# Kernel tuning notes

Measured on AMD Instinct MI355X. Metric: run time of the kernel, lower is better.

## Reference

```python
import jax, jax.numpy as jnp
import numpy as np
import math

STRIDES = [4, 8, 16, 32, 64]
SCALES  = [32, 64, 128, 256, 512]
RATIOS  = [2.0, 1.0, 0.5]
GRIDS   = [(200, 304), (100, 152), (50, 76), (25, 38), (13, 19)]  # 800x1216 canvas
LSZ     = [gh * gw * 3 for gh, gw in GRIDS]                        # anchors per level
PRE_NMS_K = [min(1000, n) for n in LSZ]                            # select_by_score (1000, lsz)
IMG_H, IMG_W = 800, 1216
BBOX_CLAMP = math.log(1000.0 / 16.0)
IOU_TH = 0.7
MAX_OUT = 1000
MIN_SIZE = 1e-2
LEVEL_OFFSET = 1e4  # batched-NMS level separation offset


def _make_priors():
    # post.get_priors with loc='corner': anchor centers at stride*i (no +0.5)
    out = []
    for st, (gh, gw), sc in zip(STRIDES, GRIDS, SCALES):
        anc = []
        for r in RATIOS:  # make_anchors_rounded: 1 scale x 3 ratios, rounded
            h = sc * np.sqrt(r)
            w = sc / np.sqrt(r)
            anc.append(np.round(np.array([-w / 2, -h / 2, w / 2, h / 2])))
        anc = np.stack(anc)  # [3,4]
        ys = (np.arange(gh) * st).astype(np.float32)
        xs = (np.arange(gw) * st).astype(np.float32)
        yy, xx = np.meshgrid(ys, xs, indexing='ij')
        shifts = np.stack([xx, yy, xx, yy], axis=-1).reshape(-1, 1, 4)  # [gh*gw,1,4]
        out.append((shifts + anc[None].astype(np.float32)).reshape(-1, 4))
    return np.concatenate(out).astype(np.float32)  # [A,4]


def setup_inputs() -> dict:
    key = jax.random.key(0)
    k1, k2 = jax.random.split(key)
    B, A = 16, sum(LSZ)
    reg = jax.random.normal(k1, (B, A, 4), dtype=jnp.float32) * 0.5  # box deltas
    obj = jax.random.normal(k2, (B, A, 1), dtype=jnp.float32)        # objectness logits
    priors = jnp.asarray(_make_priors())
    return {"reg": reg, "obj": obj, "priors": priors}


def _nms(boxes, init_keep):
    # sequential NMS over score-sorted boxes; boxes already level-offset. [N,4]
    N = boxes.shape[0]
    areas = jnp.clip(boxes[:, 2] - boxes[:, 0], 0) * jnp.clip(boxes[:, 3] - boxes[:, 1], 0)
    rng = jnp.arange(N)

    def body(i, keep):
        b = boxes[i]
        xx1 = jnp.maximum(b[0], boxes[:, 0])
        yy1 = jnp.maximum(b[1], boxes[:, 1])
        xx2 = jnp.minimum(b[2], boxes[:, 2])
        yy2 = jnp.minimum(b[3], boxes[:, 3])
        inter = jnp.clip(xx2 - xx1, 0) * jnp.clip(yy2 - yy1, 0)
        iou = inter / (areas[i] + areas - inter + 1e-9)
        sup = (iou > IOU_TH) & (rng > i) & keep[i]
        return keep & ~sup

    return jax.lax.fori_loop(0, N, body, init_keep)


def reference(reg, obj, priors):
    B = reg.shape[0]
    scores = jax.nn.sigmoid(obj[..., 0])  # [B,A]

    # per-level top-k selection (select_by_score with (1000, lsz))
    off = 0
    idxs, scs, levs = [], [], []
    for l, (n, k) in enumerate(zip(LSZ, PRE_NMS_K)):
        sv, si = jax.lax.top_k(scores[:, off:off + n], k)
        idxs.append(si + off)
        scs.append(sv)
        levs.append(np.full(k, l, np.int32))
        off += n
    idx = jnp.concatenate(idxs, axis=1)       # [B,N] global anchor indices
    sc = jnp.concatenate(scs, axis=1)         # [B,N]
    levels = jnp.asarray(np.concatenate(levs))  # [N]

    reg_s = jnp.take_along_axis(reg, idx[..., None], axis=1)  # [B,N,4]
    pri_s = priors[idx]                                        # [B,N,4]

    # decode_boxes, settings=(1, 1, log(1000/16))
    pw = pri_s[..., 2] - pri_s[..., 0]
    ph = pri_s[..., 3] - pri_s[..., 1]
    pcx = pri_s[..., 0] + 0.5 * pw
    pcy = pri_s[..., 1] + 0.5 * ph
    dx, dy = reg_s[..., 0], reg_s[..., 1]
    dw = jnp.minimum(reg_s[..., 2], BBOX_CLAMP)
    dh = jnp.minimum(reg_s[..., 3], BBOX_CLAMP)
    cx = dx * pw + pcx
    cy = dy * ph + pcy
    w = pw * jnp.exp(dw)
    h = ph * jnp.exp(dh)
    boxes = jnp.stack([cx - 0.5 * w, cy - 0.5 * h, cx + 0.5 * w, cy + 0.5 * h], axis=-1)

    # clamp_to_canvas
    boxes = jnp.stack([
        jnp.clip(boxes[..., 0], 0, IMG_W), jnp.clip(boxes[..., 1], 0, IMG_H),
        jnp.clip(boxes[..., 2], 0, IMG_W), jnp.clip(boxes[..., 3], 0, IMG_H)], axis=-1)

    # remove_small
    small_ok = ((boxes[..., 2] - boxes[..., 0]) > MIN_SIZE) & ((boxes[..., 3] - boxes[..., 1]) > MIN_SIZE)

    # global score-descending order for NMS
    order = jnp.argsort(-sc, axis=1)
    boxes = jnp.take_along_axis(boxes, order[..., None], axis=1)
    sc = jnp.take_along_axis(sc, order, axis=1)
    small_ok = jnp.take_along_axis(small_ok, order, axis=1)
    lev = jnp.take_along_axis(jnp.broadcast_to(levels, sc.shape), order, axis=1)

    # per-level batched NMS via coordinate offset; NMS decisions are non-differentiable
    boxes_off = jax.lax.stop_gradient(boxes) + lev[..., None].astype(boxes.dtype) * LEVEL_OFFSET
    keep = jax.vmap(_nms)(boxes_off, small_ok)  # [B,N] bool

    # take first MAX_OUT kept (already score-sorted), pad with zeros
    rank = jnp.cumsum(keep, axis=1) - 1
    pos = jnp.where(keep & (rank < MAX_OUT), rank, MAX_OUT)  # dump slot MAX_OUT
    out_b = jax.vmap(lambda p, b: jnp.zeros((MAX_OUT + 1, 4), b.dtype).at[p].set(b))(pos, boxes)[:, :MAX_OUT]
    out_s = jax.vmap(lambda p, s: jnp.zeros((MAX_OUT + 1,), s.dtype).at[p].set(s))(pos, sc)[:, :MAX_OUT]
    return jnp.concatenate([out_b, out_s[..., None]], axis=-1)  # [B,1000,5]
```

## Files before the change

### kernel.cpp

```cpp
#include <hip/hip_runtime.h>

typedef unsigned int u32;
typedef unsigned short u16;
typedef unsigned long long u64;

#define NB 16
#define NA 242991
#define NSEL 4741

__device__ __constant__ int c_LN[5]   = {182400, 45600, 11400, 2850, 741};
__device__ __constant__ int c_LOFF[5] = {0, 182400, 228000, 239400, 242250};
__device__ __constant__ int c_LK[5]   = {1000, 1000, 1000, 1000, 741};
__device__ __constant__ int c_SOFF[5] = {0, 1000, 2000, 3000, 4000};
__device__ __constant__ int c_CST[5]  = {0, 64, 80, 84, 85};
__device__ __constant__ int c_CCN[5]  = {64, 16, 4, 1, 1};


__device__ __forceinline__ float xla_tanhf(float x) {
#pragma clang fp contract(off)
  float t = fminf(fmaxf(x, -9.0f), 9.0f);
  float x2 = t * t;
  float p = -2.76076847742355e-16f;
  p = p * x2 + 2.00018790482477e-13f;
  p = p * x2 + -8.60467152213735e-11f;
  p = p * x2 + 5.12229709037114e-08f;
  p = p * x2 + 1.48572235717979e-05f;
  p = p * x2 + 6.37261928875436e-04f;
  p = p * x2 + 4.89352455891786e-03f;
  p = t * p;
  float q = 1.19825839466702e-06f;
  q = q * x2 + 1.18534705686654e-04f;
  q = q * x2 + 2.26843463243900e-03f;
  q = q * x2 + 4.89352518554385e-03f;
  float r = p / q;
  return (fabsf(x) < 0.0004f) ? x : r;
}

__device__ __forceinline__ float ref_sigmoid(float x) {
#pragma clang fp contract(off)
  float t = 0.5f * x;
  float th = xla_tanhf(t);
  return 0.5f + 0.5f * th;
}

__device__ __forceinline__ float xla_expf(float x) {
#pragma clang fp contract(off)
  float fx = x * 1.44269504088896341f + 0.5f;
  fx = floorf(fx);
  float tmp = fx * 0.693359375f;
  float z = fx * -2.12194440e-4f;
  float r = x - tmp;
  r = r - z;
  float r2 = r * r;
  float y = 1.9875691500e-4f;
  y = y * r + 1.3981999507e-3f;
  y = y * r + 8.3334519073e-3f;
  y = y * r + 4.1665795894e-2f;
  y = y * r + 1.6666665459e-1f;
  y = y * r + 5.0000001201e-1f;
  y = y * r2 + r;
  y = y + 1.0f;
  int k = (int)fx;
  float two_k = __uint_as_float((u32)((k + 127) << 23));
  return y * two_k;
}

__device__ __forceinline__ void chunk_map(int c, int& l, int& base, int& n) {
  if (c < 64)      { l = 0; base = c * 2850;                 n = 2850; }
  else if (c < 80) { l = 1; base = 182400 + (c - 64) * 2850; n = 2850; }
  else if (c < 84) { l = 2; base = 228000 + (c - 80) * 2850; n = 2850; }
  else if (c == 84){ l = 3; base = 239400;                   n = 2850; }
  else             { l = 4; base = 242250;                   n = 741;  }
}


__global__ void __launch_bounds__(256) k_hist(const float* __restrict__ obj,
                                              u16* __restrict__ ghist) {
  const int c = blockIdx.x, b = blockIdx.y;
  int l, base, n;
  chunk_map(c, l, base, n);
  __shared__ u32 h[4096];
  for (int i = threadIdx.x; i < 4096; i += 256) h[i] = 0;
  __syncthreads();
  const float* src = obj + (size_t)b * NA + base;
  for (int i = threadIdx.x; i < n; i += 256) {
    float s = ref_sigmoid(src[i]);
    atomicAdd(&h[__float_as_uint(s) >> 18], 1u);
  }
  __syncthreads();
  u32* gh = (u32*)(ghist + ((size_t)b * 86 + c) * 4096);
  for (int i = threadIdx.x; i < 2048; i += 256)
    gh[i] = (h[2 * i] & 0xFFFFu) | (h[2 * i + 1] << 16);
}


__global__ void __launch_bounds__(1024) k_thresh(const u16* __restrict__ ghist,
                                                 int2* __restrict__ binfo,
                                                 u32* __restrict__ ctrs) {
  const int l = blockIdx.x, b = blockIdx.y, t = threadIdx.x;
  const int K = c_LK[l];
  const int bl = b * 5 + l;
  if (t == 0) { ctrs[bl] = 0; ctrs[80 + bl] = 0; }
  __shared__ u32 scan[1024];
  __shared__ int sh_b;
  __shared__ u32 sh_G;
  u32 h0 = 0, h1 = 0, h2 = 0, h3 = 0;
  const int cs = c_CST[l], cn = c_CCN[l];
  const u16* base = ghist + (size_t)b * 86 * 4096 + 4 * t;
  for (int cc = 0; cc < cn; ++cc) {
    uint2 v = *(const uint2*)(base + (size_t)(cs + cc) * 4096);
    h0 += v.x & 0xFFFFu; h1 += v.x >> 16;
    h2 += v.y & 0xFFFFu; h3 += v.y >> 16;
  }
  u32 loc = h0 + h1 + h2 + h3;
  scan[t] = loc;
  __syncthreads();
  for (int d = 1; d < 1024; d <<= 1) {
    u32 v = (t + d < 1024) ? scan[t + d] : 0u;
    __syncthreads();
    scan[t] += v;
    __syncthreads();
  }
  u32 S = scan[t];
  u32 above = S - loc;
  if (S >= (u32)K && above < (u32)K) {
    u32 cacc = above;
    u32 cn2 = cacc + h3;
    if (cn2 >= (u32)K) { sh_b = 4 * t + 3; sh_G = cacc; }
    else {
      cacc = cn2; cn2 = cacc + h2;
      if (cn2 >= (u32)K) { sh_b = 4 * t + 2; sh_G = cacc; }
      else {
        cacc = cn2; cn2 = cacc + h1;
        if (cn2 >= (u32)K) { sh_b = 4 * t + 1; sh_G = cacc; }
        else { cacc = cn2; sh_b = 4 * t; sh_G = cacc; }
      }
    }
  }
  __syncthreads();
  if (t == 0) binfo[bl] = make_int2(sh_b, (int)sh_G);
}


__global__ void __launch_bounds__(256) k_emit(const float* __restrict__ obj,
                                              const int2* __restrict__ binfo,
                                              u64* __restrict__ skey,
                                              u64* __restrict__ candg,
                                              u32* __restrict__ ctrs) {
  const int c = blockIdx.x, b = blockIdx.y;
  int l, base, n;
  chunk_map(c, l, base, n);
  const int bl = b * 5 + l;
  const int bstar = binfo[bl].x;
  const float* src = obj + (size_t)b * NA + base;

  __shared__ u64 bufD[2880];
  __shared__ u64 bufC[2880];
  __shared__ u32 cntD, cntC, gbD, gbC;
  if (threadIdx.x == 0) { cntD = 0; cntC = 0; }
  __syncthreads();

  const int lane = (int)threadIdx.x & 63;
  const u64 lmask_lt = (lane == 0) ? 0ull : ((~0ull) >> (64 - lane));
  const int iters = (n + 255) >> 8;
  for (int it = 0; it < iters; ++it) {
    int i = it * 256 + (int)threadIdx.x;
    bool valid = i < n;
    float s = ref_sigmoid(valid ? src[i] : 0.0f);
    u32 bits = __float_as_uint(s);
    int bin = (int)(bits >> 18);
    bool isD = valid && (bin > bstar);
    bool isC = valid && (bin == bstar);
    u64 mD = __ballot(isD);
    u64 mC = __ballot(isC);
    u32 bD = 0, bC = 0;
    if (lane == 0) {
      if (mD) bD = atomicAdd(&cntD, (u32)__popcll(mD));
      if (mC) bC = atomicAdd(&cntC, (u32)__popcll(mC));
    }
    bD = (u32)__shfl((int)bD, 0, 64);
    bC = (u32)__shfl((int)bC, 0, 64);
    u64 key = ((u64)(bits ^ 0xFFFFFFFFu) << 32) | (u32)(base + i);
    if (isD) bufD[bD + (u32)__popcll(mD & lmask_lt)] = key;
    if (isC) bufC[bC + (u32)__popcll(mC & lmask_lt)] = key;
  }
  __syncthreads();
  if (threadIdx.x == 0) {
    gbD = atomicAdd(&ctrs[bl], cntD);
    gbC = atomicAdd(&ctrs[80 + bl], cntC);
  }
  __syncthreads();
  const u32 nD = cntD, nC = cntC, gD = gbD, gC = gbC;
  u64* dstD = skey + (size_t)b * NSEL + c_SOFF[l] + gD;
  for (u32 i = threadIdx.x; i < nD; i += 256) dstD[i] = bufD[i];
  u64* dstC = candg + (size_t)bl * 2048;
  for (u32 i = threadIdx.x; i < nC; i += 256) {
    u32 p = gC + i;
    if (p < 2048) dstC[p] = bufC[i];
  }
}


__device__ __forceinline__ u64 shflx64(u64 v, int d) {
  u32 lo = (u32)v, hi = (u32)(v >> 32);
  lo = (u32)__shfl_xor((int)lo, d, 64);
  hi = (u32)__shfl_xor((int)hi, d, 64);
  return ((u64)hi << 32) | (u64)lo;
}

__global__ void __launch_bounds__(1024) k_selsort(
    const u64* __restrict__ candg, const int2* __restrict__ binfo,
    const u32* __restrict__ ctrs, u64* __restrict__ skey,
    const float* __restrict__ reg, const float* __restrict__ priors,
    float* __restrict__ boxes, float* __restrict__ scoref,
    float* __restrict__ nmsbox, u64* __restrict__ sow) {
  const int l = blockIdx.x, b = blockIdx.y, t = threadIdx.x;
  const int bl = b * 5 + l;
  const int K = c_LK[l];
  const int G = binfo[bl].y;
  u32 cc = ctrs[80 + bl];
  if (cc > 2048) cc = 2048;
  __shared__ u64 sm[4096];
  __shared__ u64 sh_sow[16];
  if (t < 16) sh_sow[t] = 0ull;
  const u64* seg = skey + (size_t)b * NSEL + c_SOFF[l];
  const u64* cnd = candg + (size_t)bl * 2048;

  const int i0 = 4 * t;
  auto ld = [&](int i) -> u64 {
    if (i < G) return seg[i];
    int ci = i - G;
    return (ci < (int)cc) ? cnd[ci] : ~0ull;
  };
  u64 v0 = ld(i0), v1 = ld(i0 + 1), v2 = ld(i0 + 2), v3 = ld(i0 + 3);

  auto cs = [](u64& a, u64& b2, bool up) {
    if ((a > b2) == up) { u64 x = a; a = b2; b2 = x; }
  };

  cs(v0, v1, true);
  cs(v2, v3, false);
  {
    bool up = ((i0 & 4) == 0);
    cs(v0, v2, up); cs(v1, v3, up);
    cs(v0, v1, up); cs(v2, v3, up);
  }
  for (int k = 8; k <= 4096; k <<= 1) {
    const bool up = ((i0 & k) == 0);
    for (int j = k >> 1; j >= 256; j >>= 1) {
      sm[t] = v0; sm[1024 + t] = v1; sm[2048 + t] = v2; sm[3072 + t] = v3;
      __syncthreads();
      const int u = t ^ (j >> 2);
      u64 o0 = sm[u], o1 = sm[1024 + u], o2 = sm[2048 + u], o3 = sm[3072 + u];
      const bool keepmin = (((i0 & j) == 0) == up);
      v0 = keepmin ? (v0 < o0 ? v0 : o0) : (v0 > o0 ? v0 : o0);
      v1 = keepmin ? (v1 < o1 ? v1 : o1) : (v1 > o1 ? v1 : o1);
      v2 = keepmin ? (v2 < o2 ? v2 : o2) : (v2 > o2 ? v2 : o2);
      v3 = keepmin ? (v3 < o3 ? v3 : o3) : (v3 > o3 ? v3 : o3);
      __syncthreads();
    }
    int jstart = (k >> 1) < 128 ? (k >> 1) : 128;
    for (int j = jstart; j >= 4; j >>= 1) {
      const int d = j >> 2;
      const bool keepmin = (((t & d) == 0) == up);
      u64 o0 = shflx64(v0, d);
      u64 o1 = shflx64(v1, d);
      u64 o2 = shflx64(v2, d);
      u64 o3 = shflx64(v3, d);
      v0 = keepmin ? (v0 < o0 ? v0 : o0) : (v0 > o0 ? v0 : o0);
      v1 = keepmin ? (v1 < o1 ? v1 : o1) : (v1 > o1 ? v1 : o1);
      v2 = keepmin ? (v2 < o2 ? v2 : o2) : (v2 > o2 ? v2 : o2);
      v3 = keepmin ? (v3 < o3 ? v3 : o3) : (v3 > o3 ? v3 : o3);
    }
    cs(v0, v2, up); cs(v1, v3, up);
    cs(v0, v1, up); cs(v2, v3, up);
  }

  u64* dst = skey + (size_t)b * NSEL + c_SOFF[l];

  {
#pragma clang fp contract(off)
    const float lf = (float)l * 10000.0f;
    u64 kv[4] = {v0, v1, v2, v3};
#pragma unroll
    for (int e = 0; e < 4; ++e) {
      int r = i0 + e;
      if (r < K) {
        u64 kk = kv[e];
        dst[r] = kk;
        u32 idx = (u32)kk;
        if (idx >= (u32)NA) idx = NA - 1;
        u32 bits = (u32)(kk >> 32) ^ 0xFFFFFFFFu;
        float s = __uint_as_float(bits);
        float4 r4 = ((const float4*)reg)[(size_t)b * NA + idx];
        float4 q4 = ((const float4*)priors)[idx];
        float pw = q4.z - q4.x;
        float ph = q4.w - q4.y;
        float pcx = q4.x + 0.5f * pw;
        float pcy = q4.y + 0.5f * ph;
        float dw = fminf(r4.z, 4.135166556742356f);
        float dh = fminf(r4.w, 4.135166556742356f);
        float cx = r4.x * pw + pcx;
        float cy = r4.y * ph + pcy;
        float w = pw * xla_expf(dw);
        float h = ph * xla_expf(dh);
        float x1 = cx - 0.5f * w;
        float y1 = cy - 0.5f * h;
        float x2 = cx + 0.5f * w;
        float y2 = cy + 0.5f * h;
        x1 = fminf(fmaxf(x1, 0.0f), 1216.0f);
        y1 = fminf(fmaxf(y1, 0.0f), 800.0f);
        x2 = fminf(fmaxf(x2, 0.0f), 1216.0f);
        y2 = fminf(fmaxf(y2, 0.0f), 800.0f);
        bool ok = ((x2 - x1) > 0.01f) && ((y2 - y1) > 0.01f);
        int sidx = c_SOFF[l] + r;
        ((float4*)boxes)[(size_t)b * NSEL + sidx] = make_float4(x1, y1, x2, y2);
        scoref[(size_t)b * NSEL + sidx] = s;
        ((float4*)nmsbox)[(size_t)(b * 5 + l) * 1000 + r] =
            make_float4(x1 + lf, y1 + lf, x2 + lf, y2 + lf);
        if (ok) atomicOr(&sh_sow[r >> 6], 1ull << (r & 63));
      }
    }
  }
  __syncthreads();
  if (t < 16) sow[(size_t)b * 80 + l * 16 + t] = sh_sow[t];
}


__device__ __forceinline__ void tile_map(int k, int& l, int& ti, int& tj) {
  int W;
  if (k < 544) { l = k / 136; k -= l * 136; W = 16; }
  else         { l = 4; k -= 544; W = 12; }
  int a = 0;
  while (k >= W - a) { k -= W - a; a++; }
  ti = a; tj = a + k;
}

__global__ void __launch_bounds__(256) k_nms_build(const float* __restrict__ nmsbox,
                                                   u64* __restrict__ mk) {
#pragma clang fp contract(off)
  const int b = blockIdx.y;
  const int wv = (int)threadIdx.x >> 6;
  const int tid = blockIdx.x * 4 + wv;
  __shared__ float4 cbox[4][64];
  __shared__ float car[4][64];
  if (tid >= 622) return;
  const int lane = (int)threadIdx.x & 63;
  int l, ti, tj;
  tile_map(tid, l, ti, tj);
  const int N = c_LK[l];
  const int bl = b * 5 + l;
  const float4* src = (const float4*)(nmsbox + (size_t)bl * 4000);
  const int i = ti * 64 + lane;
  const int j = tj * 64 + lane;
  const int il = (i < N) ? i : (N - 1);
  const int jl = (j < N) ? j : (N - 1);
  float4 rb = src[il];
  float4 cb0 = src[jl];
  float ra = fmaxf(rb.z - rb.x, 0.0f) * fmaxf(rb.w - rb.y, 0.0f);
  float ca0 = fmaxf(cb0.z - cb0.x, 0.0f) * fmaxf(cb0.w - cb0.y, 0.0f);
  cbox[wv][lane] = cb0;
  car[wv][lane] = ca0;
  u32 mlo = 0u, mhi = 0u;
  const double M = 0.7000000178813934326171875;
#pragma unroll
  for (int c = 0; c < 64; ++c) {
    float4 cb = cbox[wv][c];
    float aj = car[wv][c];
    float xx1 = fmaxf(rb.x, cb.x);
    float yy1 = fmaxf(rb.y, cb.y);
    float xx2 = fminf(rb.z, cb.z);
    float yy2 = fminf(rb.w, cb.w);
    float inter = fmaxf(xx2 - xx1, 0.0f) * fmaxf(yy2 - yy1, 0.0f);
    float den = ((ra + aj) - inter) + 1e-9f;
    bool sup = ((double)inter >= M * (double)den);
    if (c < 32) mlo |= sup ? (1u << c) : 0u;
    else        mhi |= sup ? (1u << (c - 32)) : 0u;
  }
  u64 m = ((u64)mhi << 32) | (u64)mlo;
  if (ti == tj) m &= (lane == 63) ? 0ull : (~0ull << (lane + 1));
  int nc = N - tj * 64;
  if (nc < 64) m &= (1ull << nc) - 1ull;
  if (i < N) mk[(size_t)bl * 16000 + (size_t)tj * 1000 + i] = m;
}


__global__ void __launch_bounds__(1024) k_nms_scan(const u64* __restrict__ mk,
                                                   const u64* __restrict__ sow,
                                                   u64* __restrict__ keepw) {
  const int bl = blockIdx.x;
  const int b = bl / 5, l = bl % 5;
  const int N = c_LK[l];
  const int W = (N + 63) >> 6;
  const int lane = (int)threadIdx.x & 63;
  const int w = (int)threadIdx.x >> 6;
  const bool act = (w < W);
  __shared__ u64 sh_kept[16];

  const u64* rowp = mk + (size_t)bl * 16000 + (size_t)w * 1000;
  u64 acc = act ? ~sow[(size_t)b * 80 + l * 16 + w] : 0ull;

  u64 diag = 0ull;
  if (act) {
    int rd = w * 64 + lane;
    if (rd < N) diag = rowp[rd];
  }
  u64 nxt = (act && w > 0) ? rowp[lane] : 0ull;

  for (int g = 0; g < 16; ++g) {
    if (g >= W) break;
    u64 cur = nxt;
    if (act && w > g + 1) {
      int r = (g + 1) * 64 + lane;
      nxt = (r < N) ? rowp[r] : 0ull;
    } else {
      nxt = 0ull;
    }
    if (w == g) {
      u64 sup = acc;
      u64 pend = __ballot(diag != 0) & ~sup;
      while (pend) {
        int i = __builtin_ctzll(pend);
        u64 rr = __shfl(diag, i, 64);
        sup |= rr;
        pend &= ~sup;
        pend &= ~(1ull << i);
      }
      acc = sup;
      if (lane == 0) sh_kept[g] = ~sup;
    }
    __syncthreads();
    if (act && w > g) {
      u64 K = sh_kept[g];
      u64 c = ((K >> lane) & 1ull) ? cur : 0ull;
#pragma unroll
      for (int d = 1; d < 64; d <<= 1) c |= __shfl_xor(c, d, 64);
      acc |= c;
    }
    __syncthreads();
  }
  if (act && lane == 0) keepw[(size_t)b * 80 + l * 16 + w] = ~acc;
}


__global__ void __launch_bounds__(1024) k_out(const float* __restrict__ boxes,
                                              const float* __restrict__ scoref,
                                              const u64* __restrict__ skey,
                                              const u64* __restrict__ keepw,
                                              float* __restrict__ out) {
  const int l = blockIdx.x, b = blockIdx.y, t = threadIdx.x;
  __shared__ u64 sk[NSEL];
  __shared__ u64 kw[80];
  __shared__ u32 pp[5][17];
  __shared__ u32 sh_T;
  for (int i = t; i < NSEL; i += 1024) sk[i] = skey[(size_t)b * NSEL + i];
  if (t < 80) {
    int l2 = t >> 4, w = t & 15;
    int W = (c_LK[l2] + 63) >> 6;
    kw[t] = (w < W) ? keepw[(size_t)b * 80 + t] : 0ull;
  }
  __syncthreads();
  if (t < 5) {
    u32 acc = 0;
    pp[t][0] = 0;
    for (int w = 0; w < 16; ++w) {
      acc += (u32)__popcll(kw[t * 16 + w]);
      pp[t][w + 1] = acc;
    }
  }
  __syncthreads();
  if (t == 0) sh_T = pp[0][16] + pp[1][16] + pp[2][16] + pp[3][16] + pp[4][16];
  __syncthreads();
  const u32 T = sh_T;
  const int K = c_LK[l];

  for (int r = t; r < K; r += 1024) {
    int s = c_SOFF[l] + r;
    u64 word = kw[l * 16 + (r >> 6)];
    if ((word >> (r & 63)) & 1ull) {
      u32 rank = pp[l][r >> 6] +
                 (u32)__popcll(word & ((r & 63) ? ((1ull << (r & 63)) - 1ull) : 0ull));
      u64 key = sk[s];
#pragma unroll
      for (int l2 = 0; l2 < 5; ++l2) {
        if (l2 == l) continue;
        int lo = 0, hi = c_LK[l2];
        const int base2 = c_SOFF[l2];
        while (lo < hi) {
          int mid = (lo + hi) >> 1;
          if (sk[base2 + mid] < key) lo = mid + 1; else hi = mid;
        }
        u64 w2 = kw[l2 * 16 + (lo >> 6)];
        rank += pp[l2][lo >> 6] +
                (u32)__popcll(w2 & ((lo & 63) ? ((1ull << (lo & 63)) - 1ull) : 0ull));
      }
      if (rank < 1000u) {
        float4 bo = ((const float4*)boxes)[(size_t)b * NSEL + s];
        float* o = out + ((size_t)b * 1000 + rank) * 5;
        o[0] = bo.x; o[1] = bo.y; o[2] = bo.z; o[3] = bo.w;
        o[4] = scoref[(size_t)b * NSEL + s];
      }
    }
  }
  if (l == 0) {
    u32 start = (T < 1000u) ? T : 1000u;
    for (u32 i = start + t; i < 1000u; i += 1024u) {
      float* o = out + ((size_t)b * 1000 + i) * 5;
      o[0] = 0.0f; o[1] = 0.0f; o[2] = 0.0f; o[3] = 0.0f; o[4] = 0.0f;
    }
  }
}


extern "C" void kernel_launch(void* const* d_in, const int* in_sizes, int n_in,
                              void* d_out, int out_size, void* d_ws, size_t ws_size,
                              hipStream_t stream) {
  const float* reg = (const float*)d_in[0];
  const float* obj = (const float*)d_in[1];
  const float* priors = (const float*)d_in[2];
  float* out = (float*)d_out;

  char* ws = (char*)d_ws;
  size_t off = 0;
  auto alloc = [&](size_t bytes) {
    size_t r = off;
    off += (bytes + 255) & ~(size_t)255;
    return r;
  };
  u16* ghist = (u16*)(ws + alloc((size_t)NB * 86 * 4096 * 2));
  u32* ctrs = (u32*)(ws + alloc(160 * 4));
  int2* binfo = (int2*)(ws + alloc(80 * 8));
  u64* candg = (u64*)(ws + alloc((size_t)80 * 2048 * 8));
  u64* skey = (u64*)(ws + alloc((size_t)NB * NSEL * 8));
  float* boxes = (float*)(ws + alloc((size_t)NB * NSEL * 16));
  float* scoref = (float*)(ws + alloc((size_t)NB * NSEL * 4));
  float* nmsbox = (float*)(ws + alloc((size_t)NB * 5 * 1000 * 16));
  u64* sow = (u64*)(ws + alloc((size_t)NB * 80 * 8));
  u64* keepw = (u64*)(ws + alloc((size_t)NB * 80 * 8));
  u64* mk = (u64*)(ws + alloc((size_t)80 * 1000 * 16 * 8));

  k_hist<<<dim3(86, NB), 256, 0, stream>>>(obj, ghist);
  k_thresh<<<dim3(5, NB), 1024, 0, stream>>>(ghist, binfo, ctrs);
  k_emit<<<dim3(86, NB), 256, 0, stream>>>(obj, binfo, skey, candg, ctrs);
  k_selsort<<<dim3(5, NB), 1024, 0, stream>>>(candg, binfo, ctrs, skey, reg,
                                              priors, boxes, scoref, nmsbox, sow);
  k_nms_build<<<dim3(156, NB), 256, 0, stream>>>(nmsbox, mk);
  k_nms_scan<<<dim3(80), 1024, 0, stream>>>(mk, sow, keepw);
  k_out<<<dim3(5, NB), 1024, 0, stream>>>(boxes, scoref, skey, keepw, out);
}
```

Before: 120.8 us.

## Pack emit counters, shrink bitonic sort size, skip non-overlapping IoU columns

The emit kernel packs the D and C per-wave counts into a single 16/16-bit shared atomic, so there is one LDS atomic per wave iteration instead of two. The selection sort now picks a 2048-element network when the candidates fit, which idles half the threads and drops one merge stage. The NMS mask kernel skips the double-precision IoU test for any column where no lane in the wave has a positive intersection. The packed counters assume per-block counts stay below 65536, and the wave-uniform branch adds a ballot for every column.

```diff
diff --git a/kernel.cpp b/kernel.cpp
--- a/kernel.cpp
+++ b/kernel.cpp
@@ -156,8 +156,8 @@
 
   __shared__ u64 bufD[2880];
   __shared__ u64 bufC[2880];
-  __shared__ u32 cntD, cntC, gbD, gbC;
-  if (threadIdx.x == 0) { cntD = 0; cntC = 0; }
+  __shared__ u32 cntDC, gbD, gbC;
+  if (threadIdx.x == 0) cntDC = 0;
   __syncthreads();
 
   const int lane = (int)threadIdx.x & 63;
@@ -173,24 +173,24 @@
     bool isC = valid && (bin == bstar);
     u64 mD = __ballot(isD);
     u64 mC = __ballot(isC);
-    u32 bD = 0, bC = 0;
+    u32 bDC = 0;
     if (lane == 0) {
-      if (mD) bD = atomicAdd(&cntD, (u32)__popcll(mD));
-      if (mC) bC = atomicAdd(&cntC, (u32)__popcll(mC));
-    }
-    bD = (u32)__shfl((int)bD, 0, 64);
-    bC = (u32)__shfl((int)bC, 0, 64);
+      u32 add = (u32)__popcll(mD) | ((u32)__popcll(mC) << 16);
+      if (add) bDC = atomicAdd(&cntDC, add);
+    }
+    bDC = (u32)__shfl((int)bDC, 0, 64);
     u64 key = ((u64)(bits ^ 0xFFFFFFFFu) << 32) | (u32)(base + i);
-    if (isD) bufD[bD + (u32)__popcll(mD & lmask_lt)] = key;
-    if (isC) bufC[bC + (u32)__popcll(mC & lmask_lt)] = key;
-  }
-  __syncthreads();
+    if (isD) bufD[(bDC & 0xFFFFu) + (u32)__popcll(mD & lmask_lt)] = key;
+    if (isC) bufC[(bDC >> 16) + (u32)__popcll(mC & lmask_lt)] = key;
+  }
+  __syncthreads();
+  const u32 nD = cntDC & 0xFFFFu, nC = cntDC >> 16;
   if (threadIdx.x == 0) {
-    gbD = atomicAdd(&ctrs[bl], cntD);
-    gbC = atomicAdd(&ctrs[80 + bl], cntC);
-  }
-  __syncthreads();
-  const u32 nD = cntD, nC = cntC, gD = gbD, gC = gbC;
+    gbD = atomicAdd(&ctrs[bl], nD);
+    gbC = atomicAdd(&ctrs[80 + bl], nC);
+  }
+  __syncthreads();
+  const u32 gD = gbD, gC = gbC;
   u64* dstD = skey + (size_t)b * NSEL + c_SOFF[l] + gD;
   for (u32 i = threadIdx.x; i < nD; i += 256) dstD[i] = bufD[i];
   u64* dstC = candg + (size_t)bl * 2048;
@@ -226,54 +226,66 @@
   const u64* seg = skey + (size_t)b * NSEL + c_SOFF[l];
   const u64* cnd = candg + (size_t)bl * 2048;
 
+  const int total = G + (int)cc;
+  const int NS = (total <= 2048) ? 2048 : 4096;
+  const int Q = NS >> 2;
+  const bool act = (t < Q);
   const int i0 = 4 * t;
-  auto ld = [&](int i) -> u64 {
-    if (i < G) return seg[i];
-    int ci = i - G;
-    return (ci < (int)cc) ? cnd[ci] : ~0ull;
-  };
-  u64 v0 = ld(i0), v1 = ld(i0 + 1), v2 = ld(i0 + 2), v3 = ld(i0 + 3);
+
+  u64 v0 = ~0ull, v1 = ~0ull, v2 = ~0ull, v3 = ~0ull;
+  if (act) {
+    auto ld = [&](int i) -> u64 {
+      if (i < G) return seg[i];
+      int ci = i - G;
+      return (ci < (int)cc) ? cnd[ci] : ~0ull;
+    };
+    v0 = ld(i0); v1 = ld(i0 + 1); v2 = ld(i0 + 2); v3 = ld(i0 + 3);
+  }
 
   auto cs = [](u64& a, u64& b2, bool up) {
     if ((a > b2) == up) { u64 x = a; a = b2; b2 = x; }
   };
 
-  cs(v0, v1, true);
-  cs(v2, v3, false);
-  {
+  if (act) {
+    cs(v0, v1, true);
+    cs(v2, v3, false);
     bool up = ((i0 & 4) == 0);
     cs(v0, v2, up); cs(v1, v3, up);
     cs(v0, v1, up); cs(v2, v3, up);
   }
-  for (int k = 8; k <= 4096; k <<= 1) {
+  for (int k = 8; k <= NS; k <<= 1) {
     const bool up = ((i0 & k) == 0);
     for (int j = k >> 1; j >= 256; j >>= 1) {
-      sm[t] = v0; sm[1024 + t] = v1; sm[2048 + t] = v2; sm[3072 + t] = v3;
+      if (act) { sm[t] = v0; sm[Q + t] = v1; sm[2 * Q + t] = v2; sm[3 * Q + t] = v3; }
       __syncthreads();
-      const int u = t ^ (j >> 2);
-      u64 o0 = sm[u], o1 = sm[1024 + u], o2 = sm[2048 + u], o3 = sm[3072 + u];
-      const bool keepmin = (((i0 & j) == 0) == up);
-      v0 = keepmin ? (v0 < o0 ? v0 : o0) : (v0 > o0 ? v0 : o0);
-      v1 = keepmin ? (v1 < o1 ? v1 : o1) : (v1 > o1 ? v1 : o1);
-      v2 = keepmin ? (v2 < o2 ? v2 : o2) : (v2 > o2 ? v2 : o2);
-      v3 = keepmin ? (v3 < o3 ? v3 : o3) : (v3 > o3 ? v3 : o3);
+      if (act) {
+        const int u = t ^ (j >> 2);
+        u64 o0 = sm[u], o1 = sm[Q + u], o2 = sm[2 * Q + u], o3 = sm[3 * Q + u];
+        const bool keepmin = (((i0 & j) == 0) == up);
+        v0 = keepmin ? (v0 < o0 ? v0 : o0) : (v0 > o0 ? v0 : o0);
+        v1 = keepmin ? (v1 < o1 ? v1 : o1) : (v1 > o1 ? v1 : o1);
+        v2 = keepmin ? (v2 < o2 ? v2 : o2) : (v2 > o2 ? v2 : o2);
+        v3 = keepmin ? (v3 < o3 ? v3 : o3) : (v3 > o3 ? v3 : o3);
+      }
       __syncthreads();
     }
-    int jstart = (k >> 1) < 128 ? (k >> 1) : 128;
-    for (int j = jstart; j >= 4; j >>= 1) {
-      const int d = j >> 2;
-      const bool keepmin = (((t & d) == 0) == up);
-      u64 o0 = shflx64(v0, d);
-      u64 o1 = shflx64(v1, d);
-      u64 o2 = shflx64(v2, d);
-      u64 o3 = shflx64(v3, d);
-      v0 = keepmin ? (v0 < o0 ? v0 : o0) : (v0 > o0 ? v0 : o0);
-      v1 = keepmin ? (v1 < o1 ? v1 : o1) : (v1 > o1 ? v1 : o1);
-      v2 = keepmin ? (v2 < o2 ? v2 : o2) : (v2 > o2 ? v2 : o2);
-      v3 = keepmin ? (v3 < o3 ? v3 : o3) : (v3 > o3 ? v3 : o3);
-    }
-    cs(v0, v2, up); cs(v1, v3, up);
-    cs(v0, v1, up); cs(v2, v3, up);
+    if (act) {
+      int jstart = (k >> 1) < 128 ? (k >> 1) : 128;
+      for (int j = jstart; j >= 4; j >>= 1) {
+        const int d = j >> 2;
+        const bool keepmin = (((t & d) == 0) == up);
+        u64 o0 = shflx64(v0, d);
+        u64 o1 = shflx64(v1, d);
+        u64 o2 = shflx64(v2, d);
+        u64 o3 = shflx64(v3, d);
+        v0 = keepmin ? (v0 < o0 ? v0 : o0) : (v0 > o0 ? v0 : o0);
+        v1 = keepmin ? (v1 < o1 ? v1 : o1) : (v1 > o1 ? v1 : o1);
+        v2 = keepmin ? (v2 < o2 ? v2 : o2) : (v2 > o2 ? v2 : o2);
+        v3 = keepmin ? (v3 < o3 ? v3 : o3) : (v3 > o3 ? v3 : o3);
+      }
+      cs(v0, v2, up); cs(v1, v3, up);
+      cs(v0, v1, up); cs(v2, v3, up);
+    }
   }
 
   u64* dst = skey + (size_t)b * NSEL + c_SOFF[l];
@@ -366,16 +378,18 @@
 #pragma unroll
   for (int c = 0; c < 64; ++c) {
     float4 cb = cbox[wv][c];
-    float aj = car[wv][c];
     float xx1 = fmaxf(rb.x, cb.x);
     float yy1 = fmaxf(rb.y, cb.y);
     float xx2 = fminf(rb.z, cb.z);
     float yy2 = fminf(rb.w, cb.w);
     float inter = fmaxf(xx2 - xx1, 0.0f) * fmaxf(yy2 - yy1, 0.0f);
-    float den = ((ra + aj) - inter) + 1e-9f;
-    bool sup = ((double)inter >= M * (double)den);
-    if (c < 32) mlo |= sup ? (1u << c) : 0u;
-    else        mhi |= sup ? (1u << (c - 32)) : 0u;
+    if (__any(inter > 0.0f)) {
+      float aj = car[wv][c];
+      float den = ((ra + aj) - inter) + 1e-9f;
+      bool sup = ((double)inter >= M * (double)den);
+      if (c < 32) mlo |= sup ? (1u << c) : 0u;
+      else        mhi |= sup ? (1u << (c - 32)) : 0u;
+    }
   }
   u64 m = ((u64)mhi << 32) | (u64)mlo;
   if (ti == tj) m &= (lane == 63) ? 0ull : (~0ull << (lane + 1));
```

Measured after the change: 112.4 us. 7.0% less time.
